# Optimization experiments

Hardware: AMD Instinct MI355X
Metric: run time of the kernel (lower is better)

## Reference

```python
import jax, jax.numpy as jnp
import numpy as np

D_IN = 1024
D_OUT = 1024
SEQ = 4096


def setup_inputs() -> dict:
    key = jax.random.key(0)
    k0, k1, k2, k3 = jax.random.split(key, 4)
    inputs = jax.random.normal(k0, (SEQ, D_IN), dtype=jnp.float32)
    # original uses torch.rand (uniform [0,1)) for weights
    W_q = jax.random.uniform(k1, (D_IN, D_OUT), dtype=jnp.float32)
    W_k = jax.random.uniform(k2, (D_IN, D_OUT), dtype=jnp.float32)
    W_v = jax.random.uniform(k3, (D_IN, D_OUT), dtype=jnp.float32)
    return {"inputs": inputs, "W_q": W_q, "W_k": W_k, "W_v": W_v}


def reference(inputs, W_q, W_k, W_v):
    queries = inputs @ W_q            # [S, d_out]
    keys = inputs @ W_k               # [S, d_out]
    values = inputs @ W_v             # [S, d_out]
    d_k = keys.shape[-1]
    scale = 1.0 / jnp.sqrt(jnp.asarray(d_k, dtype=queries.dtype))
    attn_scores = queries @ keys.T    # [S, S]
    attn_weights = jax.nn.softmax(attn_scores * scale, axis=-1)
    context_vectors = attn_weights @ values  # [S, d_out]
    return context_vectors
```

## Files before the change

kernel.cpp:

```cpp
#include <hip/hip_runtime.h>

typedef unsigned short u16;
typedef __attribute__((ext_vector_type(8))) short bf16x8;
typedef __attribute__((ext_vector_type(4))) float f32x4;

#define SEQ 4096
#define DIM 1024

__device__ __forceinline__ u16 f2bf(float f) {
  unsigned u = __float_as_uint(f);
  return (u16)((u + 0x7fffu + ((u >> 16) & 1u)) >> 16);
}
__device__ __forceinline__ float bf2f(u16 h) {
  return __uint_as_float(((unsigned)h) << 16);
}

__device__ __forceinline__ void gload_lds16(const void* g, void* l) {
  __builtin_amdgcn_global_load_lds(
      (const __attribute__((address_space(1))) void*)g,
      (__attribute__((address_space(3))) void*)l, 16, 0, 0);
}

__device__ __forceinline__ size_t pkoff(int row, int col, int kd) {
  int tile = (row >> 7) * (kd >> 5) + (col >> 5);
  int r7 = row & 127, c5 = col & 31;
  int slot = ((r7 >> 4) << 6) | ((c5 >> 3) << 4) | (r7 & 15);
  return (size_t)tile * 4096 + (size_t)(slot * 8 + (c5 & 7));
}

__device__ __forceinline__ void stage_tile_pk(const u16* __restrict__ g,
                                              u16* lds, int tid) {
  const int w = tid >> 6;
  gload_lds16(g + (size_t)tid * 8, lds + (size_t)(w * 64) * 8);
  gload_lds16(g + (size_t)(256 + tid) * 8, lds + (size_t)(256 + w * 64) * 8);
}

__device__ __forceinline__ void gemm3_db(
    const u16* A0, const u16* A1, const u16* B0, const u16* B1,
    int nkb, u16* lds, f32x4 (&acc)[4][4]) {
  const int tid = threadIdx.x;
  const int w = tid >> 6, l = tid & 63;
  const int wm = w >> 1, wn = w & 1;

#pragma unroll
  for (int mi = 0; mi < 4; ++mi)
#pragma unroll
    for (int ni = 0; ni < 4; ++ni)
      acc[mi][ni] = (f32x4){0.f, 0.f, 0.f, 0.f};

  const int ao = wm * 2048 + l * 8;
  const int bo = wn * 2048 + l * 8;

  stage_tile_pk(A0, lds, tid);
  stage_tile_pk(B0, lds + 4096, tid);
  stage_tile_pk(A1, lds + 8192, tid);
  stage_tile_pk(B1, lds + 12288, tid);

  for (int kb = 0; kb < nkb; ++kb) {
    __syncthreads();
    if (kb + 1 < nkb) {
      u16* nb = lds + ((kb + 1) & 1) * 16384;
      const size_t off = (size_t)(kb + 1) * 4096;
      stage_tile_pk(A0 + off, nb, tid);
      stage_tile_pk(B0 + off, nb + 4096, tid);
      stage_tile_pk(A1 + off, nb + 8192, tid);
      stage_tile_pk(B1 + off, nb + 12288, tid);
    }
    const u16* cb = lds + (kb & 1) * 16384;
    const u16* lA0 = cb;
    const u16* lB0 = cb + 4096;
    const u16* lA1 = cb + 8192;
    const u16* lB1 = cb + 12288;

    bf16x8 a0[4], b0[4];
#pragma unroll
    for (int i = 0; i < 4; ++i) {
      a0[i] = *(const bf16x8*)(lA0 + ao + i * 512);
      b0[i] = *(const bf16x8*)(lB0 + bo + i * 512);
    }
#pragma unroll
    for (int mi = 0; mi < 4; ++mi)
#pragma unroll
      for (int ni = 0; ni < 4; ++ni)
        acc[mi][ni] = __builtin_amdgcn_mfma_f32_16x16x32_bf16(
            a0[mi], b0[ni], acc[mi][ni], 0, 0, 0);
    bf16x8 b1[4];
#pragma unroll
    for (int i = 0; i < 4; ++i) b1[i] = *(const bf16x8*)(lB1 + bo + i * 512);
#pragma unroll
    for (int mi = 0; mi < 4; ++mi)
#pragma unroll
      for (int ni = 0; ni < 4; ++ni)
        acc[mi][ni] = __builtin_amdgcn_mfma_f32_16x16x32_bf16(
            a0[mi], b1[ni], acc[mi][ni], 0, 0, 0);
    bf16x8 a1[4];
#pragma unroll
    for (int i = 0; i < 4; ++i) a1[i] = *(const bf16x8*)(lA1 + ao + i * 512);
#pragma unroll
    for (int mi = 0; mi < 4; ++mi)
#pragma unroll
      for (int ni = 0; ni < 4; ++ni)
        acc[mi][ni] = __builtin_amdgcn_mfma_f32_16x16x32_bf16(
            a1[mi], b0[ni], acc[mi][ni], 0, 0, 0);
  }
  __syncthreads();
}

__device__ __forceinline__ void gemm1_db(
    const u16* A, const u16* B, int nkb, u16* lds, f32x4 (&acc)[4][4]) {
  const int tid = threadIdx.x;
  const int w = tid >> 6, l = tid & 63;
  const int wm = w >> 1, wn = w & 1;

#pragma unroll
  for (int mi = 0; mi < 4; ++mi)
#pragma unroll
    for (int ni = 0; ni < 4; ++ni)
      acc[mi][ni] = (f32x4){0.f, 0.f, 0.f, 0.f};

  const int ao = wm * 2048 + l * 8;
  const int bo = wn * 2048 + l * 8;
  const int nit = nkb >> 1;

  stage_tile_pk(A, lds, tid);
  stage_tile_pk(A + 4096, lds + 4096, tid);
  stage_tile_pk(B, lds + 8192, tid);
  stage_tile_pk(B + 4096, lds + 12288, tid);

  for (int it = 0; it < nit; ++it) {
    __syncthreads();
    if (it + 1 < nit) {
      u16* nb = lds + ((it + 1) & 1) * 16384;
      const size_t off = (size_t)(it + 1) * 8192;
      stage_tile_pk(A + off, nb, tid);
      stage_tile_pk(A + off + 4096, nb + 4096, tid);
      stage_tile_pk(B + off, nb + 8192, tid);
      stage_tile_pk(B + off + 4096, nb + 12288, tid);
    }
    const u16* cb = lds + (it & 1) * 16384;
#pragma unroll
    for (int ht = 0; ht < 2; ++ht) {
      bf16x8 av[4], bv[4];
#pragma unroll
      for (int i = 0; i < 4; ++i) {
        av[i] = *(const bf16x8*)(cb + ht * 4096 + ao + i * 512);
        bv[i] = *(const bf16x8*)(cb + 8192 + ht * 4096 + bo + i * 512);
      }
#pragma unroll
      for (int mi = 0; mi < 4; ++mi)
#pragma unroll
        for (int ni = 0; ni < 4; ++ni)
          acc[mi][ni] = __builtin_amdgcn_mfma_f32_16x16x32_bf16(
              av[mi], bv[ni], acc[mi][ni], 0, 0, 0);
    }
  }
  __syncthreads();
}

#define EPILOGUE_IDX                                          \
  const int tid = threadIdx.x, w = tid >> 6, l = tid & 63;    \
  const int wm = w >> 1, wn = w & 1, lr = l & 15, q = l >> 4; \
  (void)tid;

__device__ __forceinline__ void epilogue_pack(
    f32x4 (&acc)[4][4], u16* lds, int row0, int col0, int kd,
    u16* __restrict__ H, u16* __restrict__ L) {
  const int tid = threadIdx.x, w = tid >> 6, l = tid & 63;
  const int wm = w >> 1, wn = w & 1, lr = l & 15, q = l >> 4;
  float* lC = (float*)lds;
#pragma unroll
  for (int hh = 0; hh < 2; ++hh) {
    if (wm == hh) {
#pragma unroll
      for (int mi = 0; mi < 4; ++mi)
#pragma unroll
        for (int ni = 0; ni < 4; ++ni)
#pragma unroll
          for (int r = 0; r < 4; ++r)
            lC[(mi * 16 + q * 4 + r) * 132 + wn * 64 + ni * 16 + lr] =
                acc[mi][ni][r];
    }
    __syncthreads();
#pragma unroll
    for (int j = 0; j < 2; ++j) {
      int c = tid + 256 * j;
      int row = c >> 3, c0 = (c & 7) * 16;
      u16 hbuf[16], lbuf[16];
#pragma unroll
      for (int i = 0; i < 16; ++i) {
        float v = lC[row * 132 + c0 + i];
        u16 hv = f2bf(v);
        hbuf[i] = hv;
        lbuf[i] = f2bf(v - bf2f(hv));
      }
      int rg = row0 + hh * 64 + row;
      size_t o0 = pkoff(rg, col0 + c0, kd);
      size_t o1 = pkoff(rg, col0 + c0 + 8, kd);
      *(bf16x8*)(H + o0) = *(bf16x8*)(hbuf);
      *(bf16x8*)(H + o1) = *(bf16x8*)(hbuf + 8);
      if (L) {
        *(bf16x8*)(L + o0) = *(bf16x8*)(lbuf);
        *(bf16x8*)(L + o1) = *(bf16x8*)(lbuf + 8);
      }
    }
    if (hh == 0) __syncthreads();
  }
}


__global__ __launch_bounds__(256) void prep_kernel(
    const float* __restrict__ X,
    const float* __restrict__ W0, const float* __restrict__ W1, const float* __restrict__ W2,
    u16* __restrict__ Xh, u16* __restrict__ Xl,
    u16* __restrict__ H0, u16* __restrict__ L0,
    u16* __restrict__ H1, u16* __restrict__ L1,
    u16* __restrict__ H2) {
  const int z = blockIdx.z;
  const int tx = threadIdx.x, ty = threadIdx.y;
  if (z == 0) {
    int idx = (blockIdx.y * 32 + blockIdx.x) * 256 + ty * 32 + tx;
    int row = idx >> 6;
    int c0 = (idx & 63) * 16;
    u16 h[16], lo[16];
#pragma unroll
    for (int j = 0; j < 4; ++j) {
      float4 x = *(const float4*)(X + (size_t)row * DIM + c0 + j * 4);
      float v;
      v = x.x; h[j*4+0] = f2bf(v); lo[j*4+0] = f2bf(v - bf2f(h[j*4+0]));
      v = x.y; h[j*4+1] = f2bf(v); lo[j*4+1] = f2bf(v - bf2f(h[j*4+1]));
      v = x.z; h[j*4+2] = f2bf(v); lo[j*4+2] = f2bf(v - bf2f(h[j*4+2]));
      v = x.w; h[j*4+3] = f2bf(v); lo[j*4+3] = f2bf(v - bf2f(h[j*4+3]));
    }
    size_t o0 = pkoff(row, c0, DIM);
    size_t o1 = pkoff(row, c0 + 8, DIM);
    *(bf16x8*)(Xh + o0) = *(bf16x8*)(h);
    *(bf16x8*)(Xl + o0) = *(bf16x8*)(lo);
    *(bf16x8*)(Xh + o1) = *(bf16x8*)(h + 8);
    *(bf16x8*)(Xl + o1) = *(bf16x8*)(lo + 8);
    return;
  }
  __shared__ float t[32][33];
  const float* W = (z == 1) ? W0 : (z == 2) ? W1 : W2;
  u16* H = (z == 1) ? H0 : (z == 2) ? H1 : H2;
  u16* L = (z == 1) ? L0 : (z == 2) ? L1 : nullptr;
  const int i0 = blockIdx.y * 32, o0 = blockIdx.x * 32;
#pragma unroll
  for (int m = 0; m < 4; ++m)
    t[ty + 8 * m][tx] = W[(size_t)(i0 + ty + 8 * m) * DIM + o0 + tx];
  __syncthreads();
#pragma unroll
  for (int m = 0; m < 4; ++m) {
    float v = t[tx][ty + 8 * m];
    u16 h = f2bf(v);
    size_t o = pkoff(o0 + ty + 8 * m, i0 + tx, DIM);
    H[o] = h;
    if (L) L[o] = f2bf(v - bf2f(h));
  }
}

__global__ __launch_bounds__(256) void qkv_kernel(
    const u16* __restrict__ Xh, const u16* __restrict__ Xl,
    const u16* __restrict__ Wh0, const u16* __restrict__ Wl0,
    const u16* __restrict__ Wh1, const u16* __restrict__ Wl1,
    const u16* __restrict__ Wh2,
    u16* __restrict__ Qh, u16* __restrict__ Ql,
    u16* __restrict__ Kh, u16* __restrict__ Kl,
    u16* __restrict__ VT) {
  __shared__ __align__(16) u16 lds[2 * 4 * 4096];
  const int z = blockIdx.z;
  f32x4 acc[4][4];
  if (z < 2) {
    const u16* Wh = z ? Wh1 : Wh0;
    const u16* Wl = z ? Wl1 : Wl0;
    const int row0 = blockIdx.y * 128, col0 = blockIdx.x * 128;
    gemm3_db(Xh + (size_t)row0 * DIM, Xl + (size_t)row0 * DIM,
             Wh + (size_t)col0 * DIM, Wl + (size_t)col0 * DIM,
             DIM / 32, lds, acc);
    epilogue_pack(acc, lds, row0, col0, DIM, z ? Kh : Qh, z ? Kl : Ql);
  } else {
    const int row0 = blockIdx.x * 128;
    const int col0 = blockIdx.y * 128;
    gemm1_db(Wh2 + (size_t)row0 * DIM, Xh + (size_t)col0 * DIM,
             DIM / 32, lds, acc);
    epilogue_pack(acc, lds, row0, col0, SEQ, VT, nullptr);
  }
}

__global__ __launch_bounds__(256) void s_kernel(
    const u16* __restrict__ Qh, const u16* __restrict__ Ql,
    const u16* __restrict__ Kh, const u16* __restrict__ Kl,
    float* __restrict__ S) {
  __shared__ __align__(16) u16 lds[2 * 4 * 4096];
  const int row0 = blockIdx.y * 128, col0 = blockIdx.x * 128;
  f32x4 acc[4][4];
  gemm3_db(Qh + (size_t)row0 * DIM, Ql + (size_t)row0 * DIM,
           Kh + (size_t)col0 * DIM, Kl + (size_t)col0 * DIM,
           DIM / 32, lds, acc);
  EPILOGUE_IDX
  const float scale = 0.03125f;
#pragma unroll
  for (int mi = 0; mi < 4; ++mi)
#pragma unroll
    for (int ni = 0; ni < 4; ++ni)
#pragma unroll
      for (int r = 0; r < 4; ++r) {
        int row = row0 + wm * 64 + mi * 16 + q * 4 + r;
        int col = col0 + wn * 64 + ni * 16 + lr;
        S[(size_t)row * SEQ + col] = acc[mi][ni][r] * scale;
      }
}

__global__ __launch_bounds__(256) void softmax_kernel(const float* __restrict__ S,
                                                      u16* __restrict__ P) {
  const int row = blockIdx.x;
  const float* s = S + (size_t)row * SEQ;
  const int tid = threadIdx.x;
  const int c0 = tid * 16;
  float v[16];
  float mx = -3.4e38f;
#pragma unroll
  for (int j = 0; j < 4; ++j) {
    float4 x = *(const float4*)(s + c0 + j * 4);
    v[j * 4 + 0] = x.x; v[j * 4 + 1] = x.y; v[j * 4 + 2] = x.z; v[j * 4 + 3] = x.w;
    mx = fmaxf(mx, fmaxf(fmaxf(x.x, x.y), fmaxf(x.z, x.w)));
  }
#pragma unroll
  for (int off = 32; off; off >>= 1) mx = fmaxf(mx, __shfl_xor(mx, off));
  __shared__ float red[8];
  const int w = tid >> 6, l = tid & 63;
  if (l == 0) red[w] = mx;
  __syncthreads();
  mx = fmaxf(fmaxf(red[0], red[1]), fmaxf(red[2], red[3]));
  float sum = 0.f;
#pragma unroll
  for (int i = 0; i < 16; ++i) {
    v[i] = __expf(v[i] - mx);
    sum += v[i];
  }
#pragma unroll
  for (int off = 32; off; off >>= 1) sum += __shfl_xor(sum, off);
  if (l == 0) red[4 + w] = sum;
  __syncthreads();
  sum = red[4] + red[5] + red[6] + red[7];
  const float inv = 1.f / sum;
  u16 p[16];
#pragma unroll
  for (int i = 0; i < 16; ++i) p[i] = f2bf(v[i] * inv);
  *(bf16x8*)(P + pkoff(row, c0, SEQ)) = *(bf16x8*)(p);
  *(bf16x8*)(P + pkoff(row, c0 + 8, SEQ)) = *(bf16x8*)(p + 8);
}

__global__ __launch_bounds__(256) void o_kernel(const u16* __restrict__ P,
                                                const u16* __restrict__ VT,
                                                float* __restrict__ Opart) {
  __shared__ __align__(16) u16 lds[2 * 4 * 4096];
  const int z = blockIdx.z;
  const int row0 = blockIdx.y * 128, col0 = blockIdx.x * 128;
  const u16* A = P + (size_t)row0 * SEQ + (size_t)z * 64 * 4096;
  const u16* B = VT + (size_t)col0 * SEQ + (size_t)z * 64 * 4096;
  f32x4 acc[4][4];
  gemm1_db(A, B, 64, lds, acc);
  EPILOGUE_IDX
  float* O = Opart + (size_t)z * SEQ * DIM;
#pragma unroll
  for (int mi = 0; mi < 4; ++mi)
#pragma unroll
    for (int ni = 0; ni < 4; ++ni)
#pragma unroll
      for (int r = 0; r < 4; ++r) {
        int row = row0 + wm * 64 + mi * 16 + q * 4 + r;
        int col = col0 + wn * 64 + ni * 16 + lr;
        O[(size_t)row * DIM + col] = acc[mi][ni][r];
      }
}

__global__ __launch_bounds__(256) void o_reduce_kernel(const float* __restrict__ Op,
                                                       float* __restrict__ O) {
  const size_t N = (size_t)SEQ * DIM;
  size_t i = ((size_t)blockIdx.x * 256 + threadIdx.x) * 4;
  float4 a = *(const float4*)(Op + i);
  float4 b = *(const float4*)(Op + N + i);
  float4 rr;
  rr.x = a.x + b.x;
  rr.y = a.y + b.y;
  rr.z = a.z + b.z;
  rr.w = a.w + b.w;
  *(float4*)(O + i) = rr;
}

extern "C" void kernel_launch(void* const* d_in, const int* in_sizes, int n_in,
                              void* d_out, int out_size, void* d_ws, size_t ws_size,
                              hipStream_t stream) {
  const float* X = (const float*)d_in[0];
  const float* Wq = (const float*)d_in[1];
  const float* Wk = (const float*)d_in[2];
  const float* Wv = (const float*)d_in[3];

  const size_t MB = 1024 * 1024;
  char* w = (char*)d_ws;
  u16* Xh = (u16*)(w + 0 * MB);
  u16* Xl = (u16*)(w + 8 * MB);
  u16* WqhT = (u16*)(w + 16 * MB);
  u16* WqlT = (u16*)(w + 18 * MB);
  u16* WkhT = (u16*)(w + 20 * MB);
  u16* WklT = (u16*)(w + 22 * MB);
  u16* WvhT = (u16*)(w + 24 * MB);
  u16* Qh = (u16*)(w + 26 * MB);
  u16* Ql = (u16*)(w + 34 * MB);
  u16* Kh = (u16*)(w + 42 * MB);
  u16* Kl = (u16*)(w + 50 * MB);
  u16* VT = (u16*)(w + 58 * MB);
  float* S = (float*)(w + 66 * MB);
  u16* P = (u16*)(w + 26 * MB);
  float* Opart = (float*)(w + 66 * MB);

  prep_kernel<<<dim3(32, 32, 4), dim3(32, 8), 0, stream>>>(
      X, Wq, Wk, Wv, Xh, Xl, WqhT, WqlT, WkhT, WklT, WvhT);
  qkv_kernel<<<dim3(DIM / 128, SEQ / 128, 3), 256, 0, stream>>>(
      Xh, Xl, WqhT, WqlT, WkhT, WklT, WvhT, Qh, Ql, Kh, Kl, VT);
  s_kernel<<<dim3(SEQ / 128, SEQ / 128), 256, 0, stream>>>(Qh, Ql, Kh, Kl, S);
  softmax_kernel<<<SEQ, 256, 0, stream>>>(S, P);
  o_kernel<<<dim3(DIM / 128, SEQ / 128, 2), 256, 0, stream>>>(P, VT, Opart);
  o_reduce_kernel<<<(SEQ * DIM) / (256 * 4), 256, 0, stream>>>(Opart, (float*)d_out);
}
```

Before: 317.0 us.

## Deepen GEMM LDS pipeline to 4-slot ring with explicit vmcnt waits and setprio

Replaces the two-buffer LDS double buffering in both GEMM helpers with a four-slot ring at half-k granularity. Three phases are prefetched ahead, and each step uses manual s_waitcnt vmcnt/lgkmcnt plus a raw s_barrier in place of __syncthreads. MFMA blocks are wrapped in s_setprio so the math waves get issue priority. This aims to hide global-to-LDS latency better and cut barrier stalls. The hand-counted vmcnt values must match the number of outstanding loads, or the code will race.

```diff
diff --git a/kernel.cpp b/kernel.cpp
--- a/kernel.cpp
+++ b/kernel.cpp
@@ -20,6 +20,11 @@
       (const __attribute__((address_space(1))) void*)g,
       (__attribute__((address_space(3))) void*)l, 16, 0, 0);
 }
+
+#define LGKM0 asm volatile("s_waitcnt lgkmcnt(0)" ::: "memory")
+#define VMW8 asm volatile("s_waitcnt vmcnt(8)" ::: "memory")
+#define VMW4 asm volatile("s_waitcnt vmcnt(4)" ::: "memory")
+#define VMW0 asm volatile("s_waitcnt vmcnt(0)" ::: "memory")
 
 __device__ __forceinline__ size_t pkoff(int row, int col, int kd) {
   int tile = (row >> 7) * (kd >> 5) + (col >> 5);
@@ -33,6 +38,28 @@
   const int w = tid >> 6;
   gload_lds16(g + (size_t)tid * 8, lds + (size_t)(w * 64) * 8);
   gload_lds16(g + (size_t)(256 + tid) * 8, lds + (size_t)(256 + w * 64) * 8);
+}
+
+__device__ __forceinline__ void stage3_phase(const u16* A0, const u16* A1,
+                                             const u16* B0, const u16* B1,
+                                             int h, u16* lds, int tid) {
+  u16* slot = lds + (h & 3) * 8192;
+  const size_t off = (size_t)(h >> 1) * 4096;
+  if (h & 1) {
+    stage_tile_pk(A1 + off, slot, tid);
+    stage_tile_pk(B1 + off, slot + 4096, tid);
+  } else {
+    stage_tile_pk(A0 + off, slot, tid);
+    stage_tile_pk(B0 + off, slot + 4096, tid);
+  }
+}
+
+__device__ __forceinline__ void stage1_phase(const u16* A, const u16* B, int h,
+                                             u16* lds, int tid) {
+  u16* slot = lds + (h & 3) * 8192;
+  const size_t off = (size_t)h * 4096;
+  stage_tile_pk(A + off, slot, tid);
+  stage_tile_pk(B + off, slot + 4096, tid);
 }
 
 __device__ __forceinline__ void gemm3_db(
@@ -50,58 +77,62 @@
 
   const int ao = wm * 2048 + l * 8;
   const int bo = wn * 2048 + l * 8;
-
-  stage_tile_pk(A0, lds, tid);
-  stage_tile_pk(B0, lds + 4096, tid);
-  stage_tile_pk(A1, lds + 8192, tid);
-  stage_tile_pk(B1, lds + 12288, tid);
+  const int H = nkb * 2;
+
+  stage3_phase(A0, A1, B0, B1, 0, lds, tid);
+  stage3_phase(A0, A1, B0, B1, 1, lds, tid);
+  stage3_phase(A0, A1, B0, B1, 2, lds, tid);
 
   for (int kb = 0; kb < nkb; ++kb) {
-    __syncthreads();
-    if (kb + 1 < nkb) {
-      u16* nb = lds + ((kb + 1) & 1) * 16384;
-      const size_t off = (size_t)(kb + 1) * 4096;
-      stage_tile_pk(A0 + off, nb, tid);
-      stage_tile_pk(B0 + off, nb + 4096, tid);
-      stage_tile_pk(A1 + off, nb + 8192, tid);
-      stage_tile_pk(B1 + off, nb + 12288, tid);
-    }
-    const u16* cb = lds + (kb & 1) * 16384;
-    const u16* lA0 = cb;
-    const u16* lB0 = cb + 4096;
-    const u16* lA1 = cb + 8192;
-    const u16* lB1 = cb + 12288;
-
     bf16x8 a0[4], b0[4];
-#pragma unroll
-    for (int i = 0; i < 4; ++i) {
-      a0[i] = *(const bf16x8*)(lA0 + ao + i * 512);
-      b0[i] = *(const bf16x8*)(lB0 + bo + i * 512);
-    }
-#pragma unroll
-    for (int mi = 0; mi < 4; ++mi)
-#pragma unroll
-      for (int ni = 0; ni < 4; ++ni)
-        acc[mi][ni] = __builtin_amdgcn_mfma_f32_16x16x32_bf16(
-            a0[mi], b0[ni], acc[mi][ni], 0, 0, 0);
-    bf16x8 b1[4];
-#pragma unroll
-    for (int i = 0; i < 4; ++i) b1[i] = *(const bf16x8*)(lB1 + bo + i * 512);
-#pragma unroll
-    for (int mi = 0; mi < 4; ++mi)
-#pragma unroll
-      for (int ni = 0; ni < 4; ++ni)
-        acc[mi][ni] = __builtin_amdgcn_mfma_f32_16x16x32_bf16(
-            a0[mi], b1[ni], acc[mi][ni], 0, 0, 0);
-    bf16x8 a1[4];
-#pragma unroll
-    for (int i = 0; i < 4; ++i) a1[i] = *(const bf16x8*)(lA1 + ao + i * 512);
-#pragma unroll
-    for (int mi = 0; mi < 4; ++mi)
-#pragma unroll
-      for (int ni = 0; ni < 4; ++ni)
-        acc[mi][ni] = __builtin_amdgcn_mfma_f32_16x16x32_bf16(
-            a1[mi], b0[ni], acc[mi][ni], 0, 0, 0);
+    {
+      const int h = 2 * kb;
+      LGKM0;
+      if (kb + 1 < nkb) { VMW8; } else { VMW4; }
+      __builtin_amdgcn_s_barrier();
+      if (h + 3 < H) stage3_phase(A0, A1, B0, B1, h + 3, lds, tid);
+      const u16* slot = lds + (h & 3) * 8192;
+#pragma unroll
+      for (int i = 0; i < 4; ++i) {
+        a0[i] = *(const bf16x8*)(slot + ao + i * 512);
+        b0[i] = *(const bf16x8*)(slot + 4096 + bo + i * 512);
+      }
+      __builtin_amdgcn_s_setprio(1);
+#pragma unroll
+      for (int mi = 0; mi < 4; ++mi)
+#pragma unroll
+        for (int ni = 0; ni < 4; ++ni)
+          acc[mi][ni] = __builtin_amdgcn_mfma_f32_16x16x32_bf16(
+              a0[mi], b0[ni], acc[mi][ni], 0, 0, 0);
+      __builtin_amdgcn_s_setprio(0);
+    }
+    {
+      const int h = 2 * kb + 1;
+      LGKM0;
+      if (kb + 1 < nkb) { VMW8; } else { VMW0; }
+      __builtin_amdgcn_s_barrier();
+      if (h + 3 < H) stage3_phase(A0, A1, B0, B1, h + 3, lds, tid);
+      const u16* slot = lds + (h & 3) * 8192;
+      bf16x8 a1[4], b1[4];
+#pragma unroll
+      for (int i = 0; i < 4; ++i) b1[i] = *(const bf16x8*)(slot + 4096 + bo + i * 512);
+#pragma unroll
+      for (int i = 0; i < 4; ++i) a1[i] = *(const bf16x8*)(slot + ao + i * 512);
+      __builtin_amdgcn_s_setprio(1);
+#pragma unroll
+      for (int mi = 0; mi < 4; ++mi)
+#pragma unroll
+        for (int ni = 0; ni < 4; ++ni)
+          acc[mi][ni] = __builtin_amdgcn_mfma_f32_16x16x32_bf16(
+              a0[mi], b1[ni], acc[mi][ni], 0, 0, 0);
+#pragma unroll
+      for (int mi = 0; mi < 4; ++mi)
+#pragma unroll
+        for (int ni = 0; ni < 4; ++ni)
+          acc[mi][ni] = __builtin_amdgcn_mfma_f32_16x16x32_bf16(
+              a1[mi], b0[ni], acc[mi][ni], 0, 0, 0);
+      __builtin_amdgcn_s_setprio(0);
+    }
   }
   __syncthreads();
 }
@@ -120,39 +151,32 @@
 
   const int ao = wm * 2048 + l * 8;
   const int bo = wn * 2048 + l * 8;
-  const int nit = nkb >> 1;
-
-  stage_tile_pk(A, lds, tid);
-  stage_tile_pk(A + 4096, lds + 4096, tid);
-  stage_tile_pk(B, lds + 8192, tid);
-  stage_tile_pk(B + 4096, lds + 12288, tid);
-
-  for (int it = 0; it < nit; ++it) {
-    __syncthreads();
-    if (it + 1 < nit) {
-      u16* nb = lds + ((it + 1) & 1) * 16384;
-      const size_t off = (size_t)(it + 1) * 8192;
-      stage_tile_pk(A + off, nb, tid);
-      stage_tile_pk(A + off + 4096, nb + 4096, tid);
-      stage_tile_pk(B + off, nb + 8192, tid);
-      stage_tile_pk(B + off + 4096, nb + 12288, tid);
-    }
-    const u16* cb = lds + (it & 1) * 16384;
-#pragma unroll
-    for (int ht = 0; ht < 2; ++ht) {
-      bf16x8 av[4], bv[4];
-#pragma unroll
-      for (int i = 0; i < 4; ++i) {
-        av[i] = *(const bf16x8*)(cb + ht * 4096 + ao + i * 512);
-        bv[i] = *(const bf16x8*)(cb + 8192 + ht * 4096 + bo + i * 512);
-      }
-#pragma unroll
-      for (int mi = 0; mi < 4; ++mi)
-#pragma unroll
-        for (int ni = 0; ni < 4; ++ni)
-          acc[mi][ni] = __builtin_amdgcn_mfma_f32_16x16x32_bf16(
-              av[mi], bv[ni], acc[mi][ni], 0, 0, 0);
-    }
+  const int H = nkb;
+
+  stage1_phase(A, B, 0, lds, tid);
+  stage1_phase(A, B, 1, lds, tid);
+  stage1_phase(A, B, 2, lds, tid);
+
+  for (int h = 0; h < H; ++h) {
+    LGKM0;
+    if (h < H - 2) { VMW8; } else if (h == H - 2) { VMW4; } else { VMW0; }
+    __builtin_amdgcn_s_barrier();
+    if (h + 3 < H) stage1_phase(A, B, h + 3, lds, tid);
+    const u16* slot = lds + (h & 3) * 8192;
+    bf16x8 av[4], bv[4];
+#pragma unroll
+    for (int i = 0; i < 4; ++i) {
+      av[i] = *(const bf16x8*)(slot + ao + i * 512);
+      bv[i] = *(const bf16x8*)(slot + 4096 + bo + i * 512);
+    }
+    __builtin_amdgcn_s_setprio(1);
+#pragma unroll
+    for (int mi = 0; mi < 4; ++mi)
+#pragma unroll
+      for (int ni = 0; ni < 4; ++ni)
+        acc[mi][ni] = __builtin_amdgcn_mfma_f32_16x16x32_bf16(
+            av[mi], bv[ni], acc[mi][ni], 0, 0, 0);
+    __builtin_amdgcn_s_setprio(0);
   }
   __syncthreads();
 }
@@ -266,7 +290,7 @@
     u16* __restrict__ Qh, u16* __restrict__ Ql,
     u16* __restrict__ Kh, u16* __restrict__ Kl,
     u16* __restrict__ VT) {
-  __shared__ __align__(16) u16 lds[2 * 4 * 4096];
+  __shared__ __align__(16) u16 lds[4 * 8192];
   const int z = blockIdx.z;
   f32x4 acc[4][4];
   if (z < 2) {
@@ -290,7 +314,7 @@
     const u16* __restrict__ Qh, const u16* __restrict__ Ql,
     const u16* __restrict__ Kh, const u16* __restrict__ Kl,
     float* __restrict__ S) {
-  __shared__ __align__(16) u16 lds[2 * 4 * 4096];
+  __shared__ __align__(16) u16 lds[4 * 8192];
   const int row0 = blockIdx.y * 128, col0 = blockIdx.x * 128;
   f32x4 acc[4][4];
   gemm3_db(Qh + (size_t)row0 * DIM, Ql + (size_t)row0 * DIM,
@@ -353,7 +377,7 @@
 __global__ __launch_bounds__(256) void o_kernel(const u16* __restrict__ P,
                                                 const u16* __restrict__ VT,
                                                 float* __restrict__ Opart) {
-  __shared__ __align__(16) u16 lds[2 * 4 * 4096];
+  __shared__ __align__(16) u16 lds[4 * 8192];
   const int z = blockIdx.z;
   const int row0 = blockIdx.y * 128, col0 = blockIdx.x * 128;
   const u16* A = P + (size_t)row0 * SEQ + (size_t)z * 64 * 4096;
```

Result: no change. 323.2 us (+1.9%).
